# Performance work log

Hardware: AMD Instinct MI355X
Metric: run time of the kernel (lower is better)

Reference implementation:

```python
import jax, jax.numpy as jnp
import numpy as np

N, D = 8192, 256

def setup_inputs() -> dict:
    key = jax.random.key(0)
    k1, k2 = jax.random.split(key)
    data = jnp.zeros((1,), dtype=jnp.float32)  # unused by the module
    Z = jax.random.normal(k1, (N, D), dtype=jnp.float32)
    A_hat = jax.random.uniform(k2, (N, N), dtype=jnp.float32)
    return {"data": data, "Z": Z, "A_hat": A_hat}

def reference(data, Z, A_hat):
    A = A_hat.astype(jnp.float32)
    # D^{-1/2} A D^{-1/2}: diagonal matmuls are mathematically row/col scaling
    d_inv_sqrt = 1.0 / jnp.sqrt(A.sum(axis=1) + 1e-10)  # [N]
    A_norm = A * d_inv_sqrt[:, None] * d_inv_sqrt[None, :]  # [N, N]
    # cosine similarity (F.normalize uses eps=1e-12 clamp on the norm)
    z_norm = jnp.linalg.norm(Z, axis=1, keepdims=True)
    Z_n = Z / jnp.maximum(z_norm, 1e-12)
    similarity = Z_n @ Z_n.T  # [N, N]
    homo_loss = -jnp.sum(A_norm * similarity)
    hetero_loss = jnp.sum((1.0 - A_norm) * similarity)
    return (homo_loss, hetero_loss)
```

## Files before the change

### kernel.cpp

```cpp
#include <hip/hip_runtime.h>
#include <hip/hip_fp16.h>

typedef _Float16 f16x8  __attribute__((ext_vector_type(8)));
typedef _Float16 f16x4  __attribute__((ext_vector_type(4)));
typedef float    f32x16 __attribute__((ext_vector_type(16)));

constexpr int Nn = 8192;
constexpr int Dd = 256;

constexpr int BM = 256;
constexpr int KC = 1024;
constexpr int SK = 32;
constexpr int NSC = KC / SK;
constexpr int ABUF = BM * SK;
constexpr int YBUF = Dd * SK;

__global__ __launch_bounds__(256) void k_rowsum(const float* __restrict__ A,
                                                float* __restrict__ dis,
                                                float* __restrict__ rd,
                                                float* __restrict__ T) {
    if (blockIdx.x == 0 && threadIdx.x == 0) *T = 0.f;
    const int row  = blockIdx.x * 4 + (threadIdx.x >> 6);
    const int lane = threadIdx.x & 63;
    const float4* rp = reinterpret_cast<const float4*>(A + (size_t)row * Nn);
    float s = 0.f;
    #pragma unroll
    for (int i = 0; i < Nn / 256; ++i) {
        float4 v = rp[i * 64 + lane];
        s += (v.x + v.y) + (v.z + v.w);
    }
    #pragma unroll
    for (int off = 32; off > 0; off >>= 1) s += __shfl_down(s, off, 64);
    if (lane == 0) {
        float rs = s + 1e-10f;
        dis[row] = rsqrtf(rs);
        rd[row]  = sqrtf(rs);
    }
}

__global__ __launch_bounds__(256) void k_makeYt(const float* __restrict__ Z,
                                               const float* __restrict__ dis,
                                               _Float16* __restrict__ Yt,
                                               _Float16* __restrict__ Yr) {
    __shared__ float nrm[64][4];
    __shared__ _Float16 tile[Dd][72];
    const int t = threadIdx.x;
    const int r = t >> 2, q = t & 3;
    const int row = blockIdx.x * 64 + r;
    const float4* zp = reinterpret_cast<const float4*>(Z + (size_t)row * Dd + q * 64);
    float4 v[16];
    float ss = 0.f;
    #pragma unroll
    for (int i = 0; i < 16; ++i) {
        v[i] = zp[i];
        ss += v[i].x*v[i].x + v[i].y*v[i].y + v[i].z*v[i].z + v[i].w*v[i].w;
    }
    nrm[r][q] = ss;
    __syncthreads();
    const float tot   = nrm[r][0] + nrm[r][1] + nrm[r][2] + nrm[r][3];
    const float scale = dis[row] / fmaxf(sqrtf(tot), 1e-12f);
    #pragma unroll
    for (int i = 0; i < 16; ++i) {
        const int c0 = q * 64 + i * 4;
        f16x4 y = { (_Float16)(v[i].x * scale), (_Float16)(v[i].y * scale),
                    (_Float16)(v[i].z * scale), (_Float16)(v[i].w * scale) };
        tile[c0+0][r] = y[0];
        tile[c0+1][r] = y[1];
        tile[c0+2][r] = y[2];
        tile[c0+3][r] = y[3];
        *reinterpret_cast<f16x4*>(Yr + (size_t)row * Dd + c0) = y;
    }
    __syncthreads();
    int4*       dst = reinterpret_cast<int4*>(Yt + (size_t)t * Nn + blockIdx.x * 64);
    const int4* src = reinterpret_cast<const int4*>(&tile[t][0]);
    #pragma unroll
    for (int i = 0; i < 8; ++i) dst[i] = src[i];
}

__global__ __launch_bounds__(256) void k_colsum(const _Float16* __restrict__ Yt,
                                                const float* __restrict__ rd,
                                                float* __restrict__ s) {
    const int k = blockIdx.x;
    const int t = threadIdx.x;
    const _Float16* yp = Yt + (size_t)k * Nn + t * 32;
    const float*    rp = rd + t * 32;
    float acc = 0.f;
    #pragma unroll
    for (int i = 0; i < 32; ++i) acc += (float)yp[i] * rp[i];
    #pragma unroll
    for (int off = 32; off > 0; off >>= 1) acc += __shfl_down(acc, off, 64);
    __shared__ float red[4];
    if ((t & 63) == 0) red[t >> 6] = acc;
    __syncthreads();
    if (t == 0) s[k] = red[0] + red[1] + red[2] + red[3];
}

__global__ __launch_bounds__(1024, 4) void k_main(const float* __restrict__ A,
                                                  const _Float16* __restrict__ Yt,
                                                  const _Float16* __restrict__ Yr,
                                                  float* __restrict__ T) {
    __shared__ float    As[3 * ABUF];
    __shared__ _Float16 Ysm[3 * YBUF];

    const int ib = blockIdx.x & (Nn / BM - 1);
    const int jb = blockIdx.x >> 5;
    const int I0 = ib * BM;
    const int K0 = jb * KC;
    const int t   = threadIdx.x;
    const int w   = t >> 6;
    const int wm  = w >> 1;
    const int wn  = w & 1;
    const int l   = t & 63;
    const int ln  = l & 31;
    const int lkh = l >> 5;

    f32x16 acc[4];
    #pragma unroll
    for (int q = 0; q < 4; ++q) acc[q] = (f32x16)(0.f);

    #define STAGE(SC, B)                                                       \
    {   const int kc = K0 + (SC) * SK;                                         \
        const int ga = (l & 7) ^ (l >> 3);                                     \
        _Pragma("unroll")                                                      \
        for (int q = 0; q < 2; ++q) {                                          \
            const int row = q * 128 + w * 8 + (l >> 3);                        \
            __builtin_amdgcn_global_load_lds(                                  \
                (const __attribute__((address_space(1))) unsigned int*)        \
                    (A + (size_t)(I0 + row) * Nn + kc + ga * 4),               \
                (__attribute__((address_space(3))) unsigned int*)              \
                    (As + (B) * ABUF + (q * 128 + w * 8) * SK),                \
                16, 0, 0);                                                     \
        }                                                                      \
        const int gy = (l & 3) ^ ((l >> 3) & 3);                               \
        const int nr = w * 16 + (l >> 2);                                      \
        __builtin_amdgcn_global_load_lds(                                      \
            (const __attribute__((address_space(1))) unsigned int*)            \
                (Yt + (size_t)nr * Nn + kc + gy * 8),                          \
            (__attribute__((address_space(3))) unsigned int*)                  \
                (Ysm + (B) * YBUF + (w * 16) * SK),                            \
            16, 0, 0);                                                         \
    }

    STAGE(0, 0);
    STAGE(1, 1);

    for (int sc = 0; sc < NSC; ++sc) {
        if (sc + 1 < NSC) { asm volatile("s_waitcnt vmcnt(3)" ::: "memory"); }
        else              { asm volatile("s_waitcnt vmcnt(0)" ::: "memory"); }
        __builtin_amdgcn_s_barrier();
        if (sc + 2 < NSC) {
            const int b2 = (sc + 2) % 3;
            STAGE(sc + 2, b2);
        }
        const int cb = sc % 3;
        const float*    Ab = As  + cb * ABUF + (wm * 32 + ln) * SK;
        const _Float16* Yb = Ysm + cb * YBUF;
        const int r7 = ln & 7;
        f16x8 af[2];
        #pragma unroll
        for (int ks = 0; ks < 2; ++ks) {
            const int s0 = ks * 4 + lkh * 2;
            const float4 u0 = *reinterpret_cast<const float4*>(Ab + ((s0)     ^ r7) * 4);
            const float4 u1 = *reinterpret_cast<const float4*>(Ab + ((s0 + 1) ^ r7) * 4);
            af[ks] = f16x8{ (_Float16)u0.x, (_Float16)u0.y, (_Float16)u0.z, (_Float16)u0.w,
                            (_Float16)u1.x, (_Float16)u1.y, (_Float16)u1.z, (_Float16)u1.w };
        }
        #pragma unroll
        for (int tn = 0; tn < 4; ++tn) {
            const int n = wn * 128 + tn * 32 + ln;
            const _Float16* Yrow = Yb + n * SK;
            const int sw = (ln >> 1) & 3;
            #pragma unroll
            for (int ks = 0; ks < 2; ++ks) {
                const int tt = (ks * 2 + lkh) ^ sw;
                const f16x8 bf = *reinterpret_cast<const f16x8*>(Yrow + tt * 8);
                acc[tn] = __builtin_amdgcn_mfma_f32_32x32x16_f16(af[ks], bf, acc[tn], 0, 0, 0);
            }
        }
    }

    float part = 0.f;
    #pragma unroll
    for (int tn = 0; tn < 4; ++tn) {
        const int n = wn * 128 + tn * 32 + ln;
        #pragma unroll
        for (int r = 0; r < 16; ++r) {
            const int i = I0 + wm * 32 + (r & 3) + 8 * (r >> 2) + 4 * lkh;
            part += acc[tn][r] * (float)Yr[(size_t)i * Dd + n];
        }
    }
    #pragma unroll
    for (int off = 32; off > 0; off >>= 1) part += __shfl_down(part, off, 64);
    __shared__ float red[16];
    if (l == 0) red[w] = part;
    __syncthreads();
    if (threadIdx.x == 0) {
        float tt = 0.f;
        #pragma unroll
        for (int i = 0; i < 16; ++i) tt += red[i];
        atomicAdd(T, tt);
    }
}

__global__ __launch_bounds__(256) void k_final(const float* __restrict__ s,
                                               const float* __restrict__ T,
                                               float* __restrict__ out) {
    const int t = threadIdx.x;
    float v = s[t];
    float p = v * v;
    #pragma unroll
    for (int off = 32; off > 0; off >>= 1) p += __shfl_down(p, off, 64);
    __shared__ float red[4];
    if ((t & 63) == 0) red[t >> 6] = p;
    __syncthreads();
    if (t == 0) {
        const float ss = red[0] + red[1] + red[2] + red[3];
        const float Tv = *T;
        out[0] = -Tv;
        out[1] = ss - Tv;
    }
}

extern "C" void kernel_launch(void* const* d_in, const int* in_sizes, int n_in,
                              void* d_out, int out_size, void* d_ws, size_t ws_size,
                              hipStream_t stream) {
    const float* Z = (const float*)d_in[1];
    const float* A = (const float*)d_in[2];
    float* out = (float*)d_out;

    char* ws = (char*)d_ws;
    float*    dis = (float*)(ws);
    float*    rd  = (float*)(ws + 32768);
    float*    s   = (float*)(ws + 65536);
    float*    T   = (float*)(ws + 66560);
    _Float16* Yt  = (_Float16*)(ws + 131072);
    _Float16* Yr  = (_Float16*)(ws + 131072 + (size_t)Nn * Dd * 2);

    k_rowsum<<<Nn / 4, 256, 0, stream>>>(A, dis, rd, T);
    k_makeYt<<<Nn / 64, 256, 0, stream>>>(Z, dis, Yt, Yr);
    k_colsum<<<Dd, 256, 0, stream>>>(Yt, rd, s);
    k_main<<<(Nn / BM) * (Nn / KC), 1024, 0, stream>>>(A, Yt, Yr, T);
    k_final<<<1, 256, 0, stream>>>(s, T, out);
}
```

Measured before the change: 126.6 us.

## Convert A to fp16 in the row-sum pass and stream fp16 A into main GEMM

The row-sum kernel now also writes an fp16 copy of A (128 MB extra write), and the main kernel loads that fp16 copy instead of fp32 A. This halves the A bytes read in the main loop, shrinks the shared-memory A tiles and removes the per-stage fp32-to-fp16 conversions. The block-to-row mapping is reversed, likely so that recently written Af16 rows still sit in cache. The cost is an extra 128 MB global write plus a 128 MB reread, compared with a single 256 MB fp32 reread before, and wider workspace use.

```diff
diff --git a/kernel.cpp b/kernel.cpp
--- a/kernel.cpp
+++ b/kernel.cpp
@@ -15,7 +15,8 @@
 constexpr int ABUF = BM * SK;
 constexpr int YBUF = Dd * SK;
 
-__global__ __launch_bounds__(256) void k_rowsum(const float* __restrict__ A,
+__global__ __launch_bounds__(256) void k_rowcvt(const float* __restrict__ A,
+                                                _Float16* __restrict__ Af16,
                                                 float* __restrict__ dis,
                                                 float* __restrict__ rd,
                                                 float* __restrict__ T) {
@@ -23,11 +24,14 @@
     const int row  = blockIdx.x * 4 + (threadIdx.x >> 6);
     const int lane = threadIdx.x & 63;
     const float4* rp = reinterpret_cast<const float4*>(A + (size_t)row * Nn);
+    f16x4* wp = reinterpret_cast<f16x4*>(Af16 + (size_t)row * Nn);
     float s = 0.f;
     #pragma unroll
     for (int i = 0; i < Nn / 256; ++i) {
         float4 v = rp[i * 64 + lane];
         s += (v.x + v.y) + (v.z + v.w);
+        wp[i * 64 + lane] = f16x4{ (_Float16)v.x, (_Float16)v.y,
+                                   (_Float16)v.z, (_Float16)v.w };
     }
     #pragma unroll
     for (int off = 32; off > 0; off >>= 1) s += __shfl_down(s, off, 64);
@@ -95,14 +99,14 @@
     if (t == 0) s[k] = red[0] + red[1] + red[2] + red[3];
 }
 
-__global__ __launch_bounds__(1024, 4) void k_main(const float* __restrict__ A,
+__global__ __launch_bounds__(1024, 4) void k_main(const _Float16* __restrict__ Af,
                                                   const _Float16* __restrict__ Yt,
                                                   const _Float16* __restrict__ Yr,
                                                   float* __restrict__ T) {
-    __shared__ float    As[3 * ABUF];
+    __shared__ _Float16 As[3 * ABUF];
     __shared__ _Float16 Ysm[3 * YBUF];
 
-    const int ib = blockIdx.x & (Nn / BM - 1);
+    const int ib = (Nn / BM - 1) - (blockIdx.x & (Nn / BM - 1));
     const int jb = blockIdx.x >> 5;
     const int I0 = ib * BM;
     const int K0 = jb * KC;
@@ -119,23 +123,18 @@
     for (int q = 0; q < 4; ++q) acc[q] = (f32x16)(0.f);
 
     #define STAGE(SC, B)                                                       \
-    {   const int kc = K0 + (SC) * SK;                                         \
-        const int ga = (l & 7) ^ (l >> 3);                                     \
-        _Pragma("unroll")                                                      \
-        for (int q = 0; q < 2; ++q) {                                          \
-            const int row = q * 128 + w * 8 + (l >> 3);                        \
-            __builtin_amdgcn_global_load_lds(                                  \
-                (const __attribute__((address_space(1))) unsigned int*)        \
-                    (A + (size_t)(I0 + row) * Nn + kc + ga * 4),               \
-                (__attribute__((address_space(3))) unsigned int*)              \
-                    (As + (B) * ABUF + (q * 128 + w * 8) * SK),                \
-                16, 0, 0);                                                     \
-        }                                                                      \
-        const int gy = (l & 3) ^ ((l >> 3) & 3);                               \
-        const int nr = w * 16 + (l >> 2);                                      \
+    {   const int kc = SC == 0 ? K0 : K0 + (SC) * SK;                          \
+        const int rr = w * 16 + (l >> 2);                                      \
+        const int sl = (l & 3) ^ ((l >> 2) & 3);                               \
         __builtin_amdgcn_global_load_lds(                                      \
             (const __attribute__((address_space(1))) unsigned int*)            \
-                (Yt + (size_t)nr * Nn + kc + gy * 8),                          \
+                (Af + (size_t)(I0 + rr) * Nn + kc + sl * 8),                   \
+            (__attribute__((address_space(3))) unsigned int*)                  \
+                (As + (B) * ABUF + (w * 16) * SK),                             \
+            16, 0, 0);                                                         \
+        __builtin_amdgcn_global_load_lds(                                      \
+            (const __attribute__((address_space(1))) unsigned int*)            \
+                (Yt + (size_t)rr * Nn + kc + sl * 8),                          \
             (__attribute__((address_space(3))) unsigned int*)                  \
                 (Ysm + (B) * YBUF + (w * 16) * SK),                            \
             16, 0, 0);                                                         \
@@ -145,35 +144,29 @@
     STAGE(1, 1);
 
     for (int sc = 0; sc < NSC; ++sc) {
-        if (sc + 1 < NSC) { asm volatile("s_waitcnt vmcnt(3)" ::: "memory"); }
+        if (sc + 1 < NSC) { asm volatile("s_waitcnt vmcnt(2)" ::: "memory"); }
         else              { asm volatile("s_waitcnt vmcnt(0)" ::: "memory"); }
         __builtin_amdgcn_s_barrier();
-        if (sc + 2 < NSC) {
-            const int b2 = (sc + 2) % 3;
-            STAGE(sc + 2, b2);
-        }
+        if (sc + 2 < NSC) STAGE(sc + 2, (sc + 2) % 3);
+
         const int cb = sc % 3;
-        const float*    Ab = As  + cb * ABUF + (wm * 32 + ln) * SK;
+        const _Float16* Ab = As  + cb * ABUF + (wm * 32 + ln) * SK;
         const _Float16* Yb = Ysm + cb * YBUF;
-        const int r7 = ln & 7;
+        const int r3 = ln & 3;
         f16x8 af[2];
         #pragma unroll
         for (int ks = 0; ks < 2; ++ks) {
-            const int s0 = ks * 4 + lkh * 2;
-            const float4 u0 = *reinterpret_cast<const float4*>(Ab + ((s0)     ^ r7) * 4);
-            const float4 u1 = *reinterpret_cast<const float4*>(Ab + ((s0 + 1) ^ r7) * 4);
-            af[ks] = f16x8{ (_Float16)u0.x, (_Float16)u0.y, (_Float16)u0.z, (_Float16)u0.w,
-                            (_Float16)u1.x, (_Float16)u1.y, (_Float16)u1.z, (_Float16)u1.w };
+            const int s = (ks * 2 + lkh) ^ r3;
+            af[ks] = *reinterpret_cast<const f16x8*>(Ab + s * 8);
         }
         #pragma unroll
         for (int tn = 0; tn < 4; ++tn) {
             const int n = wn * 128 + tn * 32 + ln;
             const _Float16* Yrow = Yb + n * SK;
-            const int sw = (ln >> 1) & 3;
             #pragma unroll
             for (int ks = 0; ks < 2; ++ks) {
-                const int tt = (ks * 2 + lkh) ^ sw;
-                const f16x8 bf = *reinterpret_cast<const f16x8*>(Yrow + tt * 8);
+                const int s = (ks * 2 + lkh) ^ (n & 3);
+                const f16x8 bf = *reinterpret_cast<const f16x8*>(Yrow + s * 8);
                 acc[tn] = __builtin_amdgcn_mfma_f32_32x32x16_f16(af[ks], bf, acc[tn], 0, 0, 0);
             }
         }
@@ -229,16 +222,17 @@
     float* out = (float*)d_out;
 
     char* ws = (char*)d_ws;
-    float*    dis = (float*)(ws);
-    float*    rd  = (float*)(ws + 32768);
-    float*    s   = (float*)(ws + 65536);
-    float*    T   = (float*)(ws + 66560);
-    _Float16* Yt  = (_Float16*)(ws + 131072);
-    _Float16* Yr  = (_Float16*)(ws + 131072 + (size_t)Nn * Dd * 2);
-
-    k_rowsum<<<Nn / 4, 256, 0, stream>>>(A, dis, rd, T);
+    float*    dis  = (float*)(ws);
+    float*    rd   = (float*)(ws + 32768);
+    float*    s    = (float*)(ws + 65536);
+    float*    T    = (float*)(ws + 66560);
+    _Float16* Yt   = (_Float16*)(ws + 131072);
+    _Float16* Yr   = (_Float16*)(ws + 131072 + (size_t)Nn * Dd * 2);
+    _Float16* Af16 = (_Float16*)(ws + 131072 + (size_t)Nn * Dd * 4);
+
+    k_rowcvt<<<Nn / 4, 256, 0, stream>>>(A, Af16, dis, rd, T);
     k_makeYt<<<Nn / 64, 256, 0, stream>>>(Z, dis, Yt, Yr);
     k_colsum<<<Dd, 256, 0, stream>>>(Yt, rd, s);
-    k_main<<<(Nn / BM) * (Nn / KC), 1024, 0, stream>>>(A, Yt, Yr, T);
+    k_main<<<(Nn / BM) * (Nn / KC), 1024, 0, stream>>>(Af16, Yt, Yr, T);
     k_final<<<1, 256, 0, stream>>>(s, T, out);
 }
```

Measured after the change: 152.6 us. +20.5%, slower.

## Halve K-slice and deepen LDS pipeline to six buffers with five-stage prefetch

Applied to the files above, without the earlier changes.

Cuts the per-stage K slice from 32 to 16 and raises the ring buffer from 3 to 6 stages, prefetching 5 stages ahead, so more global-to-LDS loads are in flight while MFMAs run. The load mapping and LDS swizzle are redone for the narrower slice. Only half the waves now load Y, which changes the per-wave vmcnt wait counts. The cost is twice as many barriers per K chunk, each covering less MFMA work.

```diff
diff --git a/kernel.cpp b/kernel.cpp
--- a/kernel.cpp
+++ b/kernel.cpp
@@ -8,10 +8,11 @@
 constexpr int Nn = 8192;
 constexpr int Dd = 256;
 
-constexpr int BM = 256;
-constexpr int KC = 1024;
-constexpr int SK = 32;
+constexpr int BM  = 256;
+constexpr int KC  = 1024;
+constexpr int SK  = 16;
 constexpr int NSC = KC / SK;
+constexpr int NB  = 6;
 constexpr int ABUF = BM * SK;
 constexpr int YBUF = Dd * SK;
 
@@ -99,8 +100,8 @@
                                                   const _Float16* __restrict__ Yt,
                                                   const _Float16* __restrict__ Yr,
                                                   float* __restrict__ T) {
-    __shared__ float    As[3 * ABUF];
-    __shared__ _Float16 Ysm[3 * YBUF];
+    __shared__ float    As[NB * ABUF];
+    __shared__ _Float16 Ysm[NB * YBUF];
 
     const int ib = blockIdx.x & (Nn / BM - 1);
     const int jb = blockIdx.x >> 5;
@@ -120,62 +121,55 @@
 
     #define STAGE(SC, B)                                                       \
     {   const int kc = K0 + (SC) * SK;                                         \
-        const int ga = (l & 7) ^ (l >> 3);                                     \
-        _Pragma("unroll")                                                      \
-        for (int q = 0; q < 2; ++q) {                                          \
-            const int row = q * 128 + w * 8 + (l >> 3);                        \
+        {   const int rr = w * 16 + (l >> 2);                                  \
+            const int sl = (l & 3) ^ ((l >> 3) & 3);                           \
             __builtin_amdgcn_global_load_lds(                                  \
                 (const __attribute__((address_space(1))) unsigned int*)        \
-                    (A + (size_t)(I0 + row) * Nn + kc + ga * 4),               \
+                    (A + (size_t)(I0 + rr) * Nn + kc + sl * 4),                \
                 (__attribute__((address_space(3))) unsigned int*)              \
-                    (As + (B) * ABUF + (q * 128 + w * 8) * SK),                \
+                    (As + (B) * ABUF + w * 256),                               \
                 16, 0, 0);                                                     \
         }                                                                      \
-        const int gy = (l & 3) ^ ((l >> 3) & 3);                               \
-        const int nr = w * 16 + (l >> 2);                                      \
-        __builtin_amdgcn_global_load_lds(                                      \
-            (const __attribute__((address_space(1))) unsigned int*)            \
-                (Yt + (size_t)nr * Nn + kc + gy * 8),                          \
-            (__attribute__((address_space(3))) unsigned int*)                  \
-                (Ysm + (B) * YBUF + (w * 16) * SK),                            \
-            16, 0, 0);                                                         \
-    }
-
-    STAGE(0, 0);
-    STAGE(1, 1);
+        if (w < 8) {                                                           \
+            const int nr = w * 32 + (l >> 1);                                  \
+            __builtin_amdgcn_global_load_lds(                                  \
+                (const __attribute__((address_space(1))) unsigned int*)        \
+                    (Yt + (size_t)nr * Nn + kc + (l & 1) * 8),                 \
+                (__attribute__((address_space(3))) unsigned int*)              \
+                    (Ysm + (B) * YBUF + w * 512),                              \
+                16, 0, 0);                                                     \
+        }                                                                      \
+    }
+
+    #define WAITV(N) asm volatile("s_waitcnt vmcnt(" #N ")" ::: "memory")
+
+    STAGE(0, 0); STAGE(1, 1); STAGE(2, 2); STAGE(3, 3); STAGE(4, 4);
 
     for (int sc = 0; sc < NSC; ++sc) {
-        if (sc + 1 < NSC) { asm volatile("s_waitcnt vmcnt(3)" ::: "memory"); }
-        else              { asm volatile("s_waitcnt vmcnt(0)" ::: "memory"); }
+        const int ah = NSC - 1 - sc;
+        if (w < 8) {
+            if (ah >= 4) WAITV(8); else if (ah == 3) WAITV(6);
+            else if (ah == 2) WAITV(4); else if (ah == 1) WAITV(2); else WAITV(0);
+        } else {
+            if (ah >= 4) WAITV(4); else if (ah == 3) WAITV(3);
+            else if (ah == 2) WAITV(2); else if (ah == 1) WAITV(1); else WAITV(0);
+        }
         __builtin_amdgcn_s_barrier();
-        if (sc + 2 < NSC) {
-            const int b2 = (sc + 2) % 3;
-            STAGE(sc + 2, b2);
-        }
-        const int cb = sc % 3;
+        if (sc + 5 < NSC) STAGE(sc + 5, (sc + 5) % NB);
+
+        const int cb = sc % NB;
         const float*    Ab = As  + cb * ABUF + (wm * 32 + ln) * SK;
         const _Float16* Yb = Ysm + cb * YBUF;
-        const int r7 = ln & 7;
-        f16x8 af[2];
-        #pragma unroll
-        for (int ks = 0; ks < 2; ++ks) {
-            const int s0 = ks * 4 + lkh * 2;
-            const float4 u0 = *reinterpret_cast<const float4*>(Ab + ((s0)     ^ r7) * 4);
-            const float4 u1 = *reinterpret_cast<const float4*>(Ab + ((s0 + 1) ^ r7) * 4);
-            af[ks] = f16x8{ (_Float16)u0.x, (_Float16)u0.y, (_Float16)u0.z, (_Float16)u0.w,
-                            (_Float16)u1.x, (_Float16)u1.y, (_Float16)u1.z, (_Float16)u1.w };
-        }
+        const int q = (ln >> 1) & 3;
+        const float4 u0 = *reinterpret_cast<const float4*>(Ab + ((lkh * 2)     ^ q) * 4);
+        const float4 u1 = *reinterpret_cast<const float4*>(Ab + ((lkh * 2 + 1) ^ q) * 4);
+        const f16x8 af = { (_Float16)u0.x, (_Float16)u0.y, (_Float16)u0.z, (_Float16)u0.w,
+                           (_Float16)u1.x, (_Float16)u1.y, (_Float16)u1.z, (_Float16)u1.w };
         #pragma unroll
         for (int tn = 0; tn < 4; ++tn) {
             const int n = wn * 128 + tn * 32 + ln;
-            const _Float16* Yrow = Yb + n * SK;
-            const int sw = (ln >> 1) & 3;
-            #pragma unroll
-            for (int ks = 0; ks < 2; ++ks) {
-                const int tt = (ks * 2 + lkh) ^ sw;
-                const f16x8 bf = *reinterpret_cast<const f16x8*>(Yrow + tt * 8);
-                acc[tn] = __builtin_amdgcn_mfma_f32_32x32x16_f16(af[ks], bf, acc[tn], 0, 0, 0);
-            }
+            const f16x8 bf = *reinterpret_cast<const f16x8*>(Yb + n * SK + lkh * 8);
+            acc[tn] = __builtin_amdgcn_mfma_f32_32x32x16_f16(af, bf, acc[tn], 0, 0, 0);
         }
     }
 
```

Result: slower. 142.9 us (+12.8%).
